# Kernel optimization log

Hardware: AMD Instinct MI355X
Metric: run time of the kernel (lower is better)

The kernel has to match this reference:

```python
import jax, jax.numpy as jnp
import numpy as np

V = 50000      # node_num
E = 200000     # number of edges
LN = 128       # feat_dim
S = 32         # stat_dim
C = 10         # num_class
T = 2          # propagation steps
MU = 0.9


def setup_inputs() -> dict:
    key = jax.random.key(0)
    ks = jax.random.split(key, 10)
    feat_Matrix = jax.random.normal(ks[0], (V, LN), dtype=jnp.float32)
    X_Node = jax.random.randint(ks[1], (E,), 0, V, dtype=jnp.int32)
    X_Neis = jax.random.randint(ks[2], (E,), 0, V, dtype=jnp.int32)
    # degrees >= 1 (divided by in Hw)
    dg_list = jax.random.randint(ks[3], (E,), 1, 33).astype(jnp.float32)
    sc = 0.02
    Wxi = jax.random.normal(ks[4], (2 * LN, S * S), dtype=jnp.float32) * sc
    bxi = jnp.zeros((S * S,), dtype=jnp.float32)
    Wrou = jax.random.normal(ks[5], (LN, S), dtype=jnp.float32) * sc
    brou = jnp.zeros((S,), dtype=jnp.float32)
    Wout = jax.random.normal(ks[6], (S, C), dtype=jnp.float32) * sc
    bout = jnp.zeros((C,), dtype=jnp.float32)
    return {
        "feat_Matrix": feat_Matrix, "X_Node": X_Node, "X_Neis": X_Neis,
        "dg_list": dg_list, "Wxi": Wxi, "bxi": bxi,
        "Wrou": Wrou, "brou": brou, "Wout": Wout, "bout": bout,
    }


def reference(feat_Matrix, X_Node, X_Neis, dg_list,
              Wxi, bxi, Wrou, brou, Wout, bout):
    # Gather endpoint features: X = [feat[u] || feat[v]]  -> [E, 2*LN]
    X = jnp.concatenate(
        (feat_Matrix[X_Node], feat_Matrix[X_Neis]), axis=1)

    # Xi(X): per-edge transition matrix A  [E, S, S], scaled by mu/s/deg
    A = jnp.tanh(X @ Wxi + bxi).reshape(E, S, S)
    A = A * (MU / S) / dg_list[:, None, None]
    # Rou on first chunk (= node features)  [E, S]
    b = jnp.tanh(X[:, :LN] @ Wrou + brou)

    H = jnp.zeros((V, S), dtype=feat_Matrix.dtype)
    for _ in range(T):
        He = H[X_Node]                                  # gather  [E, S]
        He = jnp.einsum('eij,ej->ei', A, He) + b        # per-edge transition
        # scatter-add per node (equivalent to AggrSum's dense mask matmul)
        H = jax.ops.segment_sum(He, X_Node, num_segments=V)

    # dropout is identity at inference
    return jax.nn.log_softmax(H @ Wout + bout, axis=-1)
```

## Files before the change

### kernel.cpp

```cpp
#include <hip/hip_runtime.h>

#define EE 200000
#define VV 50000
#define LN 128
#define KD 256
#define SS 32
#define NN 1024
#define CC 10
#define MUS 0.028125f

typedef short short8_t __attribute__((ext_vector_type(8)));
typedef float f32x4 __attribute__((ext_vector_type(4)));

__device__ __forceinline__ unsigned short f32_to_bf16_rne(float f) {
    union { float f; unsigned u; } x; x.f = f;
    unsigned r = x.u + 0x7FFFu + ((x.u >> 16) & 1u);
    return (unsigned short)(r >> 16);
}

__device__ __forceinline__ float bf16_to_f32(unsigned short h) {
    union { unsigned u; float f; } x; x.u = ((unsigned)h) << 16; return x.f;
}

__device__ __forceinline__ float tanh_fast(float x) {
    float t = __builtin_amdgcn_exp2f(x * 2.885390081777927f);
    return 1.0f - 2.0f * __builtin_amdgcn_rcpf(t + 1.0f);
}

__device__ __forceinline__ float ptanh(float x) {
    float x2 = x * x;
    return x * (27.f + x2) * __builtin_amdgcn_rcpf(27.f + 9.f * x2);
}

__global__ void k_hist(const int* __restrict__ Xn, int* __restrict__ cnt) {
    int e = blockIdx.x * 256 + threadIdx.x;
    if (e < EE) atomicAdd(&cnt[Xn[e]], 1);
}

__global__ void k_scan1(const int* __restrict__ cnt, int* __restrict__ rowptr,
                        int* __restrict__ bsum) {
    __shared__ int s[256];
    int i = blockIdx.x * 256 + threadIdx.x;
    int x = (i < VV) ? cnt[i] : 0;
    s[threadIdx.x] = x; __syncthreads();
    int v = x;
    #pragma unroll
    for (int off = 1; off < 256; off <<= 1) {
        int t = (threadIdx.x >= off) ? s[threadIdx.x - off] : 0;
        __syncthreads();
        v += t; s[threadIdx.x] = v;
        __syncthreads();
    }
    if (i < VV) rowptr[i] = v - x;
    if (threadIdx.x == 255) bsum[blockIdx.x] = v;
}

__global__ void k_scan2(const int* __restrict__ bsum, int* __restrict__ boff, int nb) {
    __shared__ int s[256];
    int t = threadIdx.x;
    int x = (t < nb) ? bsum[t] : 0;
    s[t] = x; __syncthreads();
    int v = x;
    #pragma unroll
    for (int off = 1; off < 256; off <<= 1) {
        int tt = (t >= off) ? s[t - off] : 0;
        __syncthreads();
        v += tt; s[t] = v;
        __syncthreads();
    }
    boff[t] = v - x;
}

__global__ void k_scan3(int* __restrict__ rowptr, const int* __restrict__ boff,
                        int* __restrict__ cursor) {
    int i = blockIdx.x * 256 + threadIdx.x;
    if (i < VV) {
        int r = rowptr[i] + boff[blockIdx.x];
        rowptr[i] = r;
        cursor[i] = r;
    }
    if (blockIdx.x == 0 && threadIdx.x == 0) rowptr[VV] = EE;
}

__global__ void k_scatter(const int* __restrict__ Xn, int* __restrict__ cursor,
                          int* __restrict__ perm) {
    int e = blockIdx.x * 256 + threadIdx.x;
    if (e < EE) {
        int p = atomicAdd(&cursor[Xn[e]], 1);
        perm[p] = e;
    }
}

__global__ void k_feat_bf16(const float* __restrict__ feat, unsigned short* __restrict__ featB) {
    int idx = blockIdx.x * 256 + threadIdx.x;
    float4 v = ((const float4*)feat)[idx];
    ushort4 o;
    o.x = f32_to_bf16_rne(v.x); o.y = f32_to_bf16_rne(v.y);
    o.z = f32_to_bf16_rne(v.z); o.w = f32_to_bf16_rne(v.w);
    ((ushort4*)featB)[idx] = o;
}

__global__ void k_wxi_bf16(const float* __restrict__ Wxi, unsigned short* __restrict__ WxiB) {
    int idx = blockIdx.x * 256 + threadIdx.x;
    int k = idx >> 10, ncol = idx & 1023;
    int np = ((ncol & 31) << 5) | (ncol >> 5);
    WxiB[((size_t)(k >> 3) * NN + np) * 8 + (k & 7)] = f32_to_bf16_rne(Wxi[idx]);
}

__global__ void k_bxiT(const float* __restrict__ bxi, float* __restrict__ bxiT) {
    int i = blockIdx.x * 256 + threadIdx.x;
    bxiT[i] = bxi[(i & 31) * 32 + (i >> 5)];
}

__global__ void k_h1(const float* __restrict__ feat, const float* __restrict__ Wrou,
                     const float* __restrict__ brou, const int* __restrict__ rowptr,
                     float* __restrict__ H1) {
    int gid = blockIdx.x * 256 + threadIdx.x;
    int u = gid >> 5, s = gid & 31;
    const float* fr = feat + (size_t)u * LN;
    float a = brou[s];
    #pragma unroll 8
    for (int k = 0; k < LN; ++k) a += fr[k] * Wrou[k * SS + s];
    float cnt = (float)(rowptr[u + 1] - rowptr[u]);
    H1[gid] = cnt * tanh_fast(a);
}

__device__ __forceinline__ void load_b(const unsigned short* __restrict__ WxiB,
                                       short8_t (&dst)[8][2], int c, int g, int l15) {
    #pragma unroll
    for (int kk = 0; kk < 8; ++kk)
        #pragma unroll
        for (int f = 0; f < 2; ++f)
            dst[kk][f] = *(const short8_t*)(WxiB +
                (size_t)((kk * 4 + g) * 1024 + c * 32 + f * 16 + l15) * 8);
}

__device__ __forceinline__ void do_mfma(const short8_t (&af)[8][2], const short8_t (&bf)[8][2],
                                        f32x4 (&acc)[2][2]) {
    #pragma unroll
    for (int kk = 0; kk < 8; ++kk)
        #pragma unroll
        for (int mf = 0; mf < 2; ++mf)
            #pragma unroll
            for (int f = 0; f < 2; ++f)
                acc[mf][f] = __builtin_amdgcn_mfma_f32_16x16x32_bf16(
                    af[kk][mf], bf[kk][f], acc[mf][f], 0, 0, 0);
}

__device__ __forceinline__ void epilogue(f32x4 (&acc)[2][2], f32x4 (&he)[2][2],
                                         const float (*hs)[33], const float* bxT,
                                         int c, int row0, int g, int l15) {
    float bx0 = bxT[c * 32 + l15];
    float bx1 = bxT[c * 32 + 16 + l15];
    #pragma unroll
    for (int mf = 0; mf < 2; ++mf)
        #pragma unroll
        for (int r = 0; r < 4; ++r) {
            float hv = hs[row0 + mf * 16 + g * 4 + r][c];
            he[mf][0][r] += ptanh(acc[mf][0][r] + bx0) * hv;
            he[mf][1][r] += ptanh(acc[mf][1][r] + bx1) * hv;
            acc[mf][0][r] = 0.f; acc[mf][1][r] = 0.f;
        }
}

__global__ void __launch_bounds__(256, 2)
k_edge_gemm(const unsigned short* __restrict__ featB, const unsigned short* __restrict__ WxiB,
            const int* __restrict__ Xn, const int* __restrict__ Xe,
            const float* __restrict__ dg, const float* __restrict__ bxiT,
            const int* __restrict__ perm, const float* __restrict__ H1,
            unsigned short* __restrict__ HeB) {
    __shared__ int   us[128], vs[128];
    __shared__ float scale_s[128];
    __shared__ float hs[128][33];
    __shared__ float bxT[1024];

    const int tid = threadIdx.x;
    const int eb = blockIdx.x * 128;

    if (tid < 128) {
        int p = eb + tid; if (p > EE - 1) p = EE - 1;
        int e0 = perm[p];
        us[tid] = Xn[e0]; vs[tid] = Xe[e0];
        scale_s[tid] = MUS / dg[e0];
    }
    #pragma unroll
    for (int it = 0; it < 4; ++it) bxT[it * 256 + tid] = bxiT[it * 256 + tid];
    __syncthreads();

    const int w = tid >> 6, lane = tid & 63;
    const int g = lane >> 4, l15 = lane & 15;
    const int row0 = w * 32;

    short8_t af[8][2];
    #pragma unroll
    for (int kk = 0; kk < 8; ++kk)
        #pragma unroll
        for (int mf = 0; mf < 2; ++mf) {
            int el = row0 + mf * 16 + l15;
            int node = (kk < 4) ? us[el] : vs[el];
            af[kk][mf] = *(const short8_t*)(featB + (size_t)node * LN + (kk & 3) * 32 + g * 8);
        }

    #pragma unroll
    for (int it = 0; it < 16; ++it) {
        int idx = it * 256 + tid;
        int el = idx >> 5, s = idx & 31;
        hs[el][s] = H1[us[el] * SS + s];
    }
    __syncthreads();

    f32x4 acc[2][2], he[2][2];
    #pragma unroll
    for (int mf = 0; mf < 2; ++mf)
        #pragma unroll
        for (int f = 0; f < 2; ++f) {
            acc[mf][f] = (f32x4){0.f, 0.f, 0.f, 0.f};
            he[mf][f]  = (f32x4){0.f, 0.f, 0.f, 0.f};
        }

    short8_t bA[8][2], bB[8][2];
    load_b(WxiB, bA, 0, g, l15);
    #pragma unroll 1
    for (int c = 0; c < 32; c += 2) {
        load_b(WxiB, bB, c + 1, g, l15);
        do_mfma(af, bA, acc);
        epilogue(acc, he, hs, bxT, c, row0, g, l15);
        load_b(WxiB, bA, (c + 2) & 31, g, l15);
        do_mfma(af, bB, acc);
        epilogue(acc, he, hs, bxT, c + 1, row0, g, l15);
    }

    #pragma unroll
    for (int mf = 0; mf < 2; ++mf)
        #pragma unroll
        for (int r = 0; r < 4; ++r) {
            int el = row0 + mf * 16 + g * 4 + r;
            int ep = eb + el;
            if (ep < EE) {
                float sc = scale_s[el];
                HeB[(size_t)ep * SS + l15]      = f32_to_bf16_rne(he[mf][0][r] * sc);
                HeB[(size_t)ep * SS + 16 + l15] = f32_to_bf16_rne(he[mf][1][r] * sc);
            }
        }
}

__global__ void k_reduce(const unsigned short* __restrict__ HeB, const int* __restrict__ rowptr,
                         const float* __restrict__ H1, float* __restrict__ H2) {
    int gid = blockIdx.x * 256 + threadIdx.x;
    int u = gid >> 5, s = gid & 31;
    int p0 = rowptr[u], p1 = rowptr[u + 1];
    float acc = H1[gid];
    for (int p = p0; p < p1; ++p)
        acc += bf16_to_f32(HeB[(size_t)p * SS + s]);
    H2[gid] = acc;
}

__global__ void k_out(const float* __restrict__ H2, const float* __restrict__ Wout,
                      const float* __restrict__ bout, float* __restrict__ out) {
    int v = blockIdx.x * 256 + threadIdx.x;
    if (v >= VV) return;
    float h[SS];
    const float4* hp = (const float4*)(H2 + (size_t)v * SS);
    #pragma unroll
    for (int q = 0; q < 8; ++q) {
        float4 t = hp[q];
        h[4*q] = t.x; h[4*q+1] = t.y; h[4*q+2] = t.z; h[4*q+3] = t.w;
    }
    float lg[CC];
    #pragma unroll
    for (int c = 0; c < CC; ++c) {
        float a = bout[c];
        #pragma unroll
        for (int s = 0; s < SS; ++s) a += h[s] * Wout[s * CC + c];
        lg[c] = a;
    }
    float mx = lg[0];
    #pragma unroll
    for (int c = 1; c < CC; ++c) mx = fmaxf(mx, lg[c]);
    float se = 0.f;
    #pragma unroll
    for (int c = 0; c < CC; ++c) se += __builtin_amdgcn_exp2f((lg[c] - mx) * 1.4426950408889634f);
    float lse = mx + __builtin_amdgcn_logf(se) * 0.6931471805599453f;
    #pragma unroll
    for (int c = 0; c < CC; ++c) out[(size_t)v * CC + c] = lg[c] - lse;
}

extern "C" void kernel_launch(void* const* d_in, const int* in_sizes, int n_in,
                              void* d_out, int out_size, void* d_ws, size_t ws_size,
                              hipStream_t stream) {
    const float* feat = (const float*)d_in[0];
    const int*   Xn   = (const int*)d_in[1];
    const int*   Xe   = (const int*)d_in[2];
    const float* dg   = (const float*)d_in[3];
    const float* Wxi  = (const float*)d_in[4];
    const float* bxi  = (const float*)d_in[5];
    const float* Wrou = (const float*)d_in[6];
    const float* brou = (const float*)d_in[7];
    const float* Wout = (const float*)d_in[8];
    const float* bout = (const float*)d_in[9];
    float* out = (float*)d_out;

    char* ws = (char*)d_ws;
    unsigned short* featB  = (unsigned short*)(ws);
    unsigned short* WxiB   = (unsigned short*)(ws + 12800000);
    unsigned short* HeB    = (unsigned short*)(ws + 13324288);
    float*          H1     = (float*)(ws + 26124288);
    float*          H2     = (float*)(ws + 32524288);
    int*            perm   = (int*)(ws + 38924288);
    int*            rowptr = (int*)(ws + 39724288);
    int*            cursor = (int*)(ws + 39924352);
    int*            cnt    = (int*)(ws + 40124352);
    int*            bsum   = (int*)(ws + 40324352);
    int*            boff   = (int*)(ws + 40325376);
    float*          bxiT   = (float*)(ws + 40326400);

    hipMemsetAsync(cnt, 0, 200000, stream);

    k_hist    <<<782, 256, 0, stream>>>(Xn, cnt);
    k_scan1   <<<196, 256, 0, stream>>>(cnt, rowptr, bsum);
    k_scan2   <<<1, 256, 0, stream>>>(bsum, boff, 196);
    k_scan3   <<<196, 256, 0, stream>>>(rowptr, boff, cursor);
    k_scatter <<<782, 256, 0, stream>>>(Xn, cursor, perm);

    k_feat_bf16<<<(VV * LN / 4) / 256, 256, 0, stream>>>(feat, featB);
    k_wxi_bf16 <<<(KD * NN) / 256, 256, 0, stream>>>(Wxi, WxiB);
    k_bxiT     <<<4, 256, 0, stream>>>(bxi, bxiT);
    k_h1       <<<(VV * SS) / 256, 256, 0, stream>>>(feat, Wrou, brou, rowptr, H1);

    k_edge_gemm<<<(EE + 127) / 128, 256, 0, stream>>>(featB, WxiB, Xn, Xe, dg, bxiT, perm, H1, HeB);

    k_reduce   <<<(VV * SS) / 256, 256, 0, stream>>>(HeB, rowptr, H1, H2);
    k_out      <<<(VV + 255) / 256, 256, 0, stream>>>(H2, Wout, bout, out);
}
```

Baseline: 376.3 us.

## Merge prep kernels, single-block scan, LDS-staged Wxi tiles, fuse reduce with output

Merges the bf16 conversions, bias transpose and histogram into one launch. Replaces the three-kernel scan with a single 1024-thread block, and has H1 read counts directly. The edge GEMM now stages Wxi tiles into LDS through global_load_lds instead of per-wave register loads, drops the bias LDS copy, and raises occupancy to 3 blocks. The reduce and log-softmax kernels are fused, removing the H2 buffer. These changes cut launch count and global traffic, at the cost of a serial scan and extra barriers in the GEMM loop.

```diff
diff --git a/kernel.cpp b/kernel.cpp
--- a/kernel.cpp
+++ b/kernel.cpp
@@ -32,54 +32,82 @@
     return x * (27.f + x2) * __builtin_amdgcn_rcpf(27.f + 9.f * x2);
 }
 
-__global__ void k_hist(const int* __restrict__ Xn, int* __restrict__ cnt) {
-    int e = blockIdx.x * 256 + threadIdx.x;
-    if (e < EE) atomicAdd(&cnt[Xn[e]], 1);
-}
-
-__global__ void k_scan1(const int* __restrict__ cnt, int* __restrict__ rowptr,
-                        int* __restrict__ bsum) {
-    __shared__ int s[256];
-    int i = blockIdx.x * 256 + threadIdx.x;
-    int x = (i < VV) ? cnt[i] : 0;
-    s[threadIdx.x] = x; __syncthreads();
-    int v = x;
-    #pragma unroll
-    for (int off = 1; off < 256; off <<= 1) {
-        int t = (threadIdx.x >= off) ? s[threadIdx.x - off] : 0;
-        __syncthreads();
-        v += t; s[threadIdx.x] = v;
-        __syncthreads();
-    }
-    if (i < VV) rowptr[i] = v - x;
-    if (threadIdx.x == 255) bsum[blockIdx.x] = v;
-}
-
-__global__ void k_scan2(const int* __restrict__ bsum, int* __restrict__ boff, int nb) {
-    __shared__ int s[256];
-    int t = threadIdx.x;
-    int x = (t < nb) ? bsum[t] : 0;
-    s[t] = x; __syncthreads();
-    int v = x;
-    #pragma unroll
-    for (int off = 1; off < 256; off <<= 1) {
-        int tt = (t >= off) ? s[t - off] : 0;
-        __syncthreads();
-        v += tt; s[t] = v;
-        __syncthreads();
-    }
-    boff[t] = v - x;
-}
-
-__global__ void k_scan3(int* __restrict__ rowptr, const int* __restrict__ boff,
-                        int* __restrict__ cursor) {
-    int i = blockIdx.x * 256 + threadIdx.x;
-    if (i < VV) {
-        int r = rowptr[i] + boff[blockIdx.x];
-        rowptr[i] = r;
-        cursor[i] = r;
-    }
-    if (blockIdx.x == 0 && threadIdx.x == 0) rowptr[VV] = EE;
+__device__ __forceinline__ void load_lds16(const void* g, void* l) {
+    __builtin_amdgcn_global_load_lds(
+        (const __attribute__((address_space(1))) unsigned int*)g,
+        (__attribute__((address_space(3))) unsigned int*)l,
+        16, 0, 0);
+}
+
+__global__ void k_prep(const float* __restrict__ feat, unsigned short* __restrict__ featB,
+                       const float* __restrict__ Wxi, unsigned short* __restrict__ WxiB,
+                       const float* __restrict__ bxi, float* __restrict__ bxiT,
+                       const int* __restrict__ Xn, int* __restrict__ cnt) {
+    int b = blockIdx.x, tid = threadIdx.x;
+    if (b < 6250) {
+        int idx = b * 256 + tid;
+        float4 v = ((const float4*)feat)[idx];
+        ushort4 o;
+        o.x = f32_to_bf16_rne(v.x); o.y = f32_to_bf16_rne(v.y);
+        o.z = f32_to_bf16_rne(v.z); o.w = f32_to_bf16_rne(v.w);
+        ((ushort4*)featB)[idx] = o;
+    } else if (b < 7274) {
+        int idx = (b - 6250) * 256 + tid;
+        int k = idx >> 10, ncol = idx & 1023;
+        int np = ((ncol & 31) << 5) | (ncol >> 5);
+        WxiB[((size_t)(k >> 3) * NN + np) * 8 + (k & 7)] = f32_to_bf16_rne(Wxi[idx]);
+    } else if (b == 7274) {
+        #pragma unroll
+        for (int it = 0; it < 4; ++it) {
+            int i = it * 256 + tid;
+            bxiT[i] = bxi[(i & 31) * 32 + (i >> 5)];
+        }
+    } else {
+        int e = (b - 7275) * 256 + tid;
+        if (e < EE) atomicAdd(&cnt[Xn[e]], 1);
+    }
+}
+
+#define SCAN_C 49
+__global__ void __launch_bounds__(1024) k_scan(const int* __restrict__ cnt,
+                                               int* __restrict__ rowptr,
+                                               int* __restrict__ cursor) {
+    __shared__ int wsum[16];
+    int tid = threadIdx.x;
+    int base = tid * SCAN_C;
+    int s = 0;
+    for (int i = 0; i < SCAN_C; ++i) {
+        int idx = base + i;
+        if (idx < VV) s += cnt[idx];
+    }
+    int lane = tid & 63, wid = tid >> 6;
+    int v = s;
+    #pragma unroll
+    for (int off = 1; off < 64; off <<= 1) {
+        int t = __shfl_up(v, off);
+        if (lane >= off) v += t;
+    }
+    if (lane == 63) wsum[wid] = v;
+    __syncthreads();
+    if (tid < 16) {
+        int x = wsum[tid];
+        #pragma unroll
+        for (int off = 1; off < 16; off <<= 1) {
+            int t = __shfl_up(x, off);
+            if (tid >= off) x += t;
+        }
+        wsum[tid] = x;
+    }
+    __syncthreads();
+    int run = v - s + (wid ? wsum[wid - 1] : 0);
+    for (int i = 0; i < SCAN_C; ++i) {
+        int idx = base + i;
+        if (idx < VV) {
+            rowptr[idx] = run; cursor[idx] = run;
+            run += cnt[idx];
+        }
+    }
+    if (tid == 0) rowptr[VV] = EE;
 }
 
 __global__ void k_scatter(const int* __restrict__ Xn, int* __restrict__ cursor,
@@ -91,29 +119,8 @@
     }
 }
 
-__global__ void k_feat_bf16(const float* __restrict__ feat, unsigned short* __restrict__ featB) {
-    int idx = blockIdx.x * 256 + threadIdx.x;
-    float4 v = ((const float4*)feat)[idx];
-    ushort4 o;
-    o.x = f32_to_bf16_rne(v.x); o.y = f32_to_bf16_rne(v.y);
-    o.z = f32_to_bf16_rne(v.z); o.w = f32_to_bf16_rne(v.w);
-    ((ushort4*)featB)[idx] = o;
-}
-
-__global__ void k_wxi_bf16(const float* __restrict__ Wxi, unsigned short* __restrict__ WxiB) {
-    int idx = blockIdx.x * 256 + threadIdx.x;
-    int k = idx >> 10, ncol = idx & 1023;
-    int np = ((ncol & 31) << 5) | (ncol >> 5);
-    WxiB[((size_t)(k >> 3) * NN + np) * 8 + (k & 7)] = f32_to_bf16_rne(Wxi[idx]);
-}
-
-__global__ void k_bxiT(const float* __restrict__ bxi, float* __restrict__ bxiT) {
-    int i = blockIdx.x * 256 + threadIdx.x;
-    bxiT[i] = bxi[(i & 31) * 32 + (i >> 5)];
-}
-
 __global__ void k_h1(const float* __restrict__ feat, const float* __restrict__ Wrou,
-                     const float* __restrict__ brou, const int* __restrict__ rowptr,
+                     const float* __restrict__ brou, const int* __restrict__ cnt,
                      float* __restrict__ H1) {
     int gid = blockIdx.x * 256 + threadIdx.x;
     int u = gid >> 5, s = gid & 31;
@@ -121,58 +128,19 @@
     float a = brou[s];
     #pragma unroll 8
     for (int k = 0; k < LN; ++k) a += fr[k] * Wrou[k * SS + s];
-    float cnt = (float)(rowptr[u + 1] - rowptr[u]);
-    H1[gid] = cnt * tanh_fast(a);
-}
-
-__device__ __forceinline__ void load_b(const unsigned short* __restrict__ WxiB,
-                                       short8_t (&dst)[8][2], int c, int g, int l15) {
-    #pragma unroll
-    for (int kk = 0; kk < 8; ++kk)
-        #pragma unroll
-        for (int f = 0; f < 2; ++f)
-            dst[kk][f] = *(const short8_t*)(WxiB +
-                (size_t)((kk * 4 + g) * 1024 + c * 32 + f * 16 + l15) * 8);
-}
-
-__device__ __forceinline__ void do_mfma(const short8_t (&af)[8][2], const short8_t (&bf)[8][2],
-                                        f32x4 (&acc)[2][2]) {
-    #pragma unroll
-    for (int kk = 0; kk < 8; ++kk)
-        #pragma unroll
-        for (int mf = 0; mf < 2; ++mf)
-            #pragma unroll
-            for (int f = 0; f < 2; ++f)
-                acc[mf][f] = __builtin_amdgcn_mfma_f32_16x16x32_bf16(
-                    af[kk][mf], bf[kk][f], acc[mf][f], 0, 0, 0);
-}
-
-__device__ __forceinline__ void epilogue(f32x4 (&acc)[2][2], f32x4 (&he)[2][2],
-                                         const float (*hs)[33], const float* bxT,
-                                         int c, int row0, int g, int l15) {
-    float bx0 = bxT[c * 32 + l15];
-    float bx1 = bxT[c * 32 + 16 + l15];
-    #pragma unroll
-    for (int mf = 0; mf < 2; ++mf)
-        #pragma unroll
-        for (int r = 0; r < 4; ++r) {
-            float hv = hs[row0 + mf * 16 + g * 4 + r][c];
-            he[mf][0][r] += ptanh(acc[mf][0][r] + bx0) * hv;
-            he[mf][1][r] += ptanh(acc[mf][1][r] + bx1) * hv;
-            acc[mf][0][r] = 0.f; acc[mf][1][r] = 0.f;
-        }
-}
-
-__global__ void __launch_bounds__(256, 2)
+    H1[gid] = (float)cnt[u] * tanh_fast(a);
+}
+
+__global__ void __launch_bounds__(256, 3)
 k_edge_gemm(const unsigned short* __restrict__ featB, const unsigned short* __restrict__ WxiB,
             const int* __restrict__ Xn, const int* __restrict__ Xe,
             const float* __restrict__ dg, const float* __restrict__ bxiT,
             const int* __restrict__ perm, const float* __restrict__ H1,
             unsigned short* __restrict__ HeB) {
+    __shared__ __align__(16) unsigned short Bs[2 * 8192];
+    __shared__ float hs[128][33];
     __shared__ int   us[128], vs[128];
     __shared__ float scale_s[128];
-    __shared__ float hs[128][33];
-    __shared__ float bxT[1024];
 
     const int tid = threadIdx.x;
     const int eb = blockIdx.x * 128;
@@ -183,8 +151,6 @@
         us[tid] = Xn[e0]; vs[tid] = Xe[e0];
         scale_s[tid] = MUS / dg[e0];
     }
-    #pragma unroll
-    for (int it = 0; it < 4; ++it) bxT[it * 256 + tid] = bxiT[it * 256 + tid];
     __syncthreads();
 
     const int w = tid >> 6, lane = tid & 63;
@@ -207,27 +173,60 @@
         int el = idx >> 5, s = idx & 31;
         hs[el][s] = H1[us[el] * SS + s];
     }
-    __syncthreads();
-
-    f32x4 acc[2][2], he[2][2];
+
+    const char* gsrc0 = (const char*)WxiB +
+        ((size_t)(((w & 1) * 16 + (lane >> 5)) * 16384) + (w >> 1) * 512 + (lane & 31) * 16);
+    char* ldst0 = (char*)Bs + w * 8192;
+    const char* bbase = (const char*)Bs + (g * 512 + l15 * 16);
+
+    f32x4 he[2][2];
     #pragma unroll
     for (int mf = 0; mf < 2; ++mf)
         #pragma unroll
-        for (int f = 0; f < 2; ++f) {
-            acc[mf][f] = (f32x4){0.f, 0.f, 0.f, 0.f};
-            he[mf][f]  = (f32x4){0.f, 0.f, 0.f, 0.f};
-        }
-
-    short8_t bA[8][2], bB[8][2];
-    load_b(WxiB, bA, 0, g, l15);
+        for (int f = 0; f < 2; ++f)
+            he[mf][f] = (f32x4){0.f, 0.f, 0.f, 0.f};
+
     #pragma unroll 1
-    for (int c = 0; c < 32; c += 2) {
-        load_b(WxiB, bB, c + 1, g, l15);
-        do_mfma(af, bA, acc);
-        epilogue(acc, he, hs, bxT, c, row0, g, l15);
-        load_b(WxiB, bA, (c + 2) & 31, g, l15);
-        do_mfma(af, bB, acc);
-        epilogue(acc, he, hs, bxT, c + 1, row0, g, l15);
+    for (int it = 0; it < 16; ++it) {
+        __syncthreads();
+        const char* gs = gsrc0 + it * 1024;
+        #pragma unroll
+        for (int q = 0; q < 8; ++q)
+            load_lds16(gs + q * 32768, ldst0 + q * 1024);
+        __syncthreads();
+
+        #pragma unroll
+        for (int ct = 0; ct < 2; ++ct) {
+            const int c = it * 2 + ct;
+            f32x4 acc[2][2];
+            #pragma unroll
+            for (int mf = 0; mf < 2; ++mf)
+                #pragma unroll
+                for (int f = 0; f < 2; ++f)
+                    acc[mf][f] = (f32x4){0.f, 0.f, 0.f, 0.f};
+
+            #pragma unroll
+            for (int kk = 0; kk < 8; ++kk) {
+                short8_t b0 = *(const short8_t*)(bbase + ct * 16384 + kk * 2048);
+                short8_t b1 = *(const short8_t*)(bbase + ct * 16384 + kk * 2048 + 256);
+                #pragma unroll
+                for (int mf = 0; mf < 2; ++mf) {
+                    acc[mf][0] = __builtin_amdgcn_mfma_f32_16x16x32_bf16(af[kk][mf], b0, acc[mf][0], 0, 0, 0);
+                    acc[mf][1] = __builtin_amdgcn_mfma_f32_16x16x32_bf16(af[kk][mf], b1, acc[mf][1], 0, 0, 0);
+                }
+            }
+
+            const float bx0 = bxiT[c * 32 + l15];
+            const float bx1 = bxiT[c * 32 + 16 + l15];
+            #pragma unroll
+            for (int mf = 0; mf < 2; ++mf)
+                #pragma unroll
+                for (int r = 0; r < 4; ++r) {
+                    float hv = hs[row0 + mf * 16 + g * 4 + r][c];
+                    he[mf][0][r] += ptanh(acc[mf][0][r] + bx0) * hv;
+                    he[mf][1][r] += ptanh(acc[mf][1][r] + bx1) * hv;
+                }
+        }
     }
 
     #pragma unroll
@@ -244,45 +243,44 @@
         }
 }
 
-__global__ void k_reduce(const unsigned short* __restrict__ HeB, const int* __restrict__ rowptr,
-                         const float* __restrict__ H1, float* __restrict__ H2) {
-    int gid = blockIdx.x * 256 + threadIdx.x;
-    int u = gid >> 5, s = gid & 31;
+__global__ void k_reduce_out(const unsigned short* __restrict__ HeB, const int* __restrict__ rowptr,
+                             const float* __restrict__ H1, const float* __restrict__ Wout,
+                             const float* __restrict__ bout, float* __restrict__ out) {
+    __shared__ float h2[8][33];
+    __shared__ float lgS[8][10];
+    __shared__ float lseS[8];
+    int tid = threadIdx.x;
+    int un8 = tid >> 5, s = tid & 31;
+    int u = blockIdx.x * 8 + un8;
     int p0 = rowptr[u], p1 = rowptr[u + 1];
-    float acc = H1[gid];
+    float acc = H1[u * SS + s];
     for (int p = p0; p < p1; ++p)
         acc += bf16_to_f32(HeB[(size_t)p * SS + s]);
-    H2[gid] = acc;
-}
-
-__global__ void k_out(const float* __restrict__ H2, const float* __restrict__ Wout,
-                      const float* __restrict__ bout, float* __restrict__ out) {
-    int v = blockIdx.x * 256 + threadIdx.x;
-    if (v >= VV) return;
-    float h[SS];
-    const float4* hp = (const float4*)(H2 + (size_t)v * SS);
-    #pragma unroll
-    for (int q = 0; q < 8; ++q) {
-        float4 t = hp[q];
-        h[4*q] = t.x; h[4*q+1] = t.y; h[4*q+2] = t.z; h[4*q+3] = t.w;
-    }
-    float lg[CC];
-    #pragma unroll
-    for (int c = 0; c < CC; ++c) {
+    h2[un8][s] = acc;
+    __syncthreads();
+    if (tid < 80) {
+        int un = tid / 10, c = tid - un * 10;
         float a = bout[c];
         #pragma unroll
-        for (int s = 0; s < SS; ++s) a += h[s] * Wout[s * CC + c];
-        lg[c] = a;
-    }
-    float mx = lg[0];
-    #pragma unroll
-    for (int c = 1; c < CC; ++c) mx = fmaxf(mx, lg[c]);
-    float se = 0.f;
-    #pragma unroll
-    for (int c = 0; c < CC; ++c) se += __builtin_amdgcn_exp2f((lg[c] - mx) * 1.4426950408889634f);
-    float lse = mx + __builtin_amdgcn_logf(se) * 0.6931471805599453f;
-    #pragma unroll
-    for (int c = 0; c < CC; ++c) out[(size_t)v * CC + c] = lg[c] - lse;
+        for (int s2 = 0; s2 < SS; ++s2) a += h2[un][s2] * Wout[s2 * CC + c];
+        lgS[un][c] = a;
+    }
+    __syncthreads();
+    if (tid < 8) {
+        float mx = lgS[tid][0];
+        #pragma unroll
+        for (int c = 1; c < CC; ++c) mx = fmaxf(mx, lgS[tid][c]);
+        float se = 0.f;
+        #pragma unroll
+        for (int c = 0; c < CC; ++c)
+            se += __builtin_amdgcn_exp2f((lgS[tid][c] - mx) * 1.4426950408889634f);
+        lseS[tid] = mx + __builtin_amdgcn_logf(se) * 0.6931471805599453f;
+    }
+    __syncthreads();
+    if (tid < 80) {
+        int un = tid / 10, c = tid - un * 10;
+        out[(size_t)(blockIdx.x * 8 + un) * CC + c] = lgS[un][c] - lseS[un];
+    }
 }
 
 extern "C" void kernel_launch(void* const* d_in, const int* in_sizes, int n_in,
@@ -305,30 +303,18 @@
     unsigned short* WxiB   = (unsigned short*)(ws + 12800000);
     unsigned short* HeB    = (unsigned short*)(ws + 13324288);
     float*          H1     = (float*)(ws + 26124288);
-    float*          H2     = (float*)(ws + 32524288);
-    int*            perm   = (int*)(ws + 38924288);
-    int*            rowptr = (int*)(ws + 39724288);
-    int*            cursor = (int*)(ws + 39924352);
-    int*            cnt    = (int*)(ws + 40124352);
-    int*            bsum   = (int*)(ws + 40324352);
-    int*            boff   = (int*)(ws + 40325376);
-    float*          bxiT   = (float*)(ws + 40326400);
+    int*            perm   = (int*)(ws + 32524288);
+    int*            rowptr = (int*)(ws + 33324288);
+    int*            cursor = (int*)(ws + 33524352);
+    int*            cnt    = (int*)(ws + 33724352);
+    float*          bxiT   = (float*)(ws + 33924352);
 
     hipMemsetAsync(cnt, 0, 200000, stream);
 
-    k_hist    <<<782, 256, 0, stream>>>(Xn, cnt);
-    k_scan1   <<<196, 256, 0, stream>>>(cnt, rowptr, bsum);
-    k_scan2   <<<1, 256, 0, stream>>>(bsum, boff, 196);
-    k_scan3   <<<196, 256, 0, stream>>>(rowptr, boff, cursor);
-    k_scatter <<<782, 256, 0, stream>>>(Xn, cursor, perm);
-
-    k_feat_bf16<<<(VV * LN / 4) / 256, 256, 0, stream>>>(feat, featB);
-    k_wxi_bf16 <<<(KD * NN) / 256, 256, 0, stream>>>(Wxi, WxiB);
-    k_bxiT     <<<4, 256, 0, stream>>>(bxi, bxiT);
-    k_h1       <<<(VV * SS) / 256, 256, 0, stream>>>(feat, Wrou, brou, rowptr, H1);
-
-    k_edge_gemm<<<(EE + 127) / 128, 256, 0, stream>>>(featB, WxiB, Xn, Xe, dg, bxiT, perm, H1, HeB);
-
-    k_reduce   <<<(VV * SS) / 256, 256, 0, stream>>>(HeB, rowptr, H1, H2);
-    k_out      <<<(VV + 255) / 256, 256, 0, stream>>>(H2, Wout, bout, out);
-}
+    k_prep      <<<8057, 256, 0, stream>>>(feat, featB, Wxi, WxiB, bxi, bxiT, Xn, cnt);
+    k_h1        <<<(VV * SS) / 256, 256, 0, stream>>>(feat, Wrou, brou, cnt, H1);
+    k_scan      <<<1, 1024, 0, stream>>>(cnt, rowptr, cursor);
+    k_scatter   <<<782, 256, 0, stream>>>(Xn, cursor, perm);
+    k_edge_gemm <<<(EE + 127) / 128, 256, 0, stream>>>(featB, WxiB, Xn, Xe, dg, bxiT, perm, H1, HeB);
+    k_reduce_out<<<VV / 8, 256, 0, stream>>>(HeB, rowptr, H1, Wout, bout, out);
+}
```

Result: slower. 425.3 us (+13.0%).
